# Optimization experiments

Measured on AMD Instinct MI355X. Metric: run time of the kernel, lower is better.

## Reference

```python
import jax, jax.numpy as jnp
import numpy as np

RMS_EPS = 1.1920928955078125e-07  # torch.finfo(float32).eps, nn.RMSNorm default when eps=None


def setup_inputs() -> dict:
    key = jax.random.key(0)
    ks = jax.random.split(key, 7)
    B, T, C, Wh, E, K = 8, 4096, 256, 1024, 8, 2
    return {
        "x": jax.random.normal(ks[0], (B, T, C), dtype=jnp.float32),
        "rms_weight": jnp.ones((C,), dtype=jnp.float32),
        "W1": jax.random.normal(ks[1], (E, C, Wh), dtype=jnp.float32),
        "b1": jax.random.normal(ks[2], (E, Wh), dtype=jnp.float32),
        "W2": jax.random.normal(ks[3], (E, Wh, C), dtype=jnp.float32),
        "b2": jax.random.normal(ks[4], (E, C), dtype=jnp.float32),
        "expert_ids": jax.random.randint(ks[5], (B, T, K), 0, E, dtype=jnp.int64),
    }


def reference(x, rms_weight, W1, b1, W2, b2, expert_ids):
    # RMSNorm over last dim (torch nn.RMSNorm, eps = float32 eps)
    xn = x * jax.lax.rsqrt(jnp.mean(x * x, axis=-1, keepdims=True) + RMS_EPS) * rms_weight
    # Per-expert 2-layer MLP. The torch code gathers per-token weight copies then bmm's;
    # mathematically identical (and far cheaper in memory) is: run every expert densely,
    # then gather the K selected expert outputs per token.
    h = jax.nn.gelu(jnp.einsum("btc,ecw->btew", xn, W1) + b1, approximate=False)  # [B,T,E,Wh]
    y = jnp.einsum("btew,ewc->btec", h, W2) + b2  # [B,T,E,C]
    # gather selected experts: [B,T,K,C]; dropout p is 0.0 (eval) -> identity
    out = jnp.take_along_axis(y, expert_ids[..., None], axis=2)
    return out
```

## Files before the change

### kernel.cpp

```cpp
#include <hip/hip_runtime.h>
#include <cstdint>

typedef unsigned short ushort_t;
typedef __bf16 bf16x8 __attribute__((ext_vector_type(8)));
typedef ushort_t u16x8 __attribute__((ext_vector_type(8)));
typedef float f32x4 __attribute__((ext_vector_type(4)));
typedef uint32_t u32x4 __attribute__((ext_vector_type(4)));

#define RMS_EPS 1.1920928955078125e-07f

__device__ __forceinline__ ushort_t f2bf(float f) {
  uint32_t u = __builtin_bit_cast(uint32_t, f);
  u += 0x7fffu + ((u >> 16) & 1u);
  return (ushort_t)(u >> 16);
}

__device__ __forceinline__ void g2l16(const ushort_t* g, ushort_t* l) {
  __builtin_amdgcn_global_load_lds(
      (const __attribute__((address_space(1))) uint32_t*)g,
      (__attribute__((address_space(3))) uint32_t*)l, 16, 0, 0);
}

__device__ __forceinline__ f32x4 mfma32(bf16x8 a, bf16x8 b, f32x4 c) {
  return __builtin_amdgcn_mfma_f32_16x16x32_bf16(a, b, c, 0, 0, 0);
}

__device__ __forceinline__ float gelu1(float v) {
  float vc = fminf(fmaxf(v, -2.9f), 2.9f);
  float x2 = vc * vc;
  float p = fmaf(-0.000414256f, x2, 0.0107517f);
  p = fmaf(p, x2, -0.1136149f);
  p = fmaf(p, x2, 0.786301f);
  float E = vc * p;
  float t = 0.5f * v;
  return fmaf(t, E, t);
}

__global__ void rmsnorm_cast(const float* __restrict__ x, const float* __restrict__ w,
                             ushort_t* __restrict__ xn) {
  int token = blockIdx.x * 4 + (threadIdx.x >> 6);
  int lane = threadIdx.x & 63;
  const float4* row = reinterpret_cast<const float4*>(x + (size_t)token * 256);
  float4 v = row[lane];
  float s = v.x * v.x + v.y * v.y + v.z * v.z + v.w * v.w;
#pragma unroll
  for (int off = 1; off < 64; off <<= 1) s += __shfl_xor(s, off);
  float inv = rsqrtf(s * (1.0f / 256.0f) + RMS_EPS);
  const float4* wr = reinterpret_cast<const float4*>(w);
  float4 wv = wr[lane];
  ushort4 o;
  o.x = f2bf(v.x * inv * wv.x);
  o.y = f2bf(v.y * inv * wv.y);
  o.z = f2bf(v.z * inv * wv.z);
  o.w = f2bf(v.w * inv * wv.w);
  *reinterpret_cast<ushort4*>(xn + (size_t)token * 256 + lane * 4) = o;
}

__global__ __launch_bounds__(256) void pack_w(const float* __restrict__ W1,
                                              const float* __restrict__ W2,
                                              ushort_t* __restrict__ w1f,
                                              ushort_t* __restrict__ w2f) {
  __shared__ ushort_t tile[64][130];
  int b = blockIdx.x;
  int isW2 = b >= 256;
  const float* src; ushort_t* dst; int e, kt, wt, rs;
  if (!isW2) { e = b >> 5; kt = (b >> 3) & 3; wt = b & 7; src = W1; dst = w1f; rs = 1024; }
  else { b -= 256; e = b >> 5; kt = (b >> 1) & 15; wt = b & 1; src = W2; dst = w2f; rs = 256; }
  int k0 = kt * 64, c0 = wt * 128;
  const float* sb = src + ((size_t)e << 18) + (size_t)k0 * rs + c0;
  int t = threadIdx.x;
#pragma unroll
  for (int i = 0; i < 8; ++i) {
    int f = i * 1024 + t * 4;
    int r = f >> 7, c = f & 127;
    float4 v = *reinterpret_cast<const float4*>(sb + (size_t)r * rs + c);
    ushort2 lo, hi;
    lo.x = f2bf(v.x); lo.y = f2bf(v.y); hi.x = f2bf(v.z); hi.y = f2bf(v.w);
    *reinterpret_cast<ushort2*>(&tile[r][c]) = lo;
    *reinterpret_cast<ushort2*>(&tile[r][c + 2]) = hi;
  }
  __syncthreads();
  int lane = t & 63, l16 = lane & 15, quad = lane >> 4;
  int wave = t >> 6;
  if (!isW2) {
#pragma unroll
    for (int p = 0; p < 4; ++p) {
      int u = p * 256 + t;
      int kk2 = (u >> 9) & 1;
      int rr = kk2 * 32 + quad * 8;
      int nt = (u >> 6) & 1, chL = (u >> 7) & 3;
      int cc = chL * 32 + nt * 16 + l16;
      u16x8 o;
#pragma unroll
      for (int j = 0; j < 8; ++j) o[j] = tile[rr + j][cc];
      size_t U = ((size_t)e * 32768) + (size_t)(wt * 4 + chL) * 1024 + (kt * 2 + kk2) * 128 + nt * 64 + lane;
      *reinterpret_cast<u16x8*>(dst + U * 8) = o;
    }
  } else {
#pragma unroll
    for (int p = 0; p < 4; ++p) {
      int u = p * 4 + wave;
      int chL = u >> 3, ctL = u & 7;
      int cc = ctL * 16 + l16;
      u16x8 o;
#pragma unroll
      for (int j = 0; j < 4; ++j) o[j] = tile[chL * 32 + quad * 4 + j][cc];
#pragma unroll
      for (int j = 0; j < 4; ++j) o[4 + j] = tile[chL * 32 + 16 + quad * 4 + j][cc];
      size_t U = (((size_t)(e * 32 + kt * 2 + chL) * 16) + (wt * 8 + ctL)) * 64 + lane;
      *reinterpret_cast<u16x8*>(dst + U * 8) = o;
    }
  }
}

__global__ void route_pairs(const int* __restrict__ eids, int* __restrict__ cnt,
                            int* __restrict__ lists) {
  __shared__ int lcnt[8], lbase[8];
  int tid = threadIdx.x;
  if (tid < 8) lcnt[tid] = 0;
  __syncthreads();
  int p = blockIdx.x * 256 + tid;
  int e = eids[p];
  int lpos = atomicAdd(&lcnt[e], 1);
  __syncthreads();
  if (tid < 8) lbase[tid] = atomicAdd(&cnt[tid], lcnt[tid]);
  __syncthreads();
  lists[e * 65536 + lbase[e] + lpos] = p;
}

__global__ __launch_bounds__(256, 3) void moe_mlp(
    const ushort_t* __restrict__ xn,
    const ushort_t* __restrict__ w1f,
    const ushort_t* __restrict__ w2f,
    const float* __restrict__ b1,
    const float* __restrict__ b2,
    const int* __restrict__ cnt,
    const int* __restrict__ lists,
    float* __restrict__ out)
{
  __shared__ __align__(16) ushort_t w1b[2][8192];
  __shared__ __align__(16) ushort_t w2b[8192];

  int nwg = gridDim.x;
  int q = nwg >> 3, r = nwg & 7;
  int xcd = blockIdx.x & 7, sub = blockIdx.x >> 3;
  int flat = (xcd < r ? xcd * (q + 1) : r * (q + 1) + (xcd - r) * q) + sub;

  int e = -1, tile = 0, accum = 0, n_e = 0;
#pragma unroll
  for (int i = 0; i < 8; ++i) {
    int c = cnt[i];
    int t = (c + 63) >> 6;
    if (e < 0 && flat < accum + t) { e = i; tile = flat - accum; n_e = c; }
    accum += t;
  }
  if (e < 0) return;
  int start = tile * 64;

  int tid = threadIdx.x;
  int wave = tid >> 6, lane = tid & 63, l16 = lane & 15, quad = lane >> 4;

  const ushort_t* w1e = w1f + ((size_t)e << 18);
  const ushort_t* w2e = w2f + ((size_t)e << 18);
  const int* le = lists + e * 65536;

  int gi = start + wave * 16 + l16;
  int pr = le[(gi < n_e) ? gi : 0];

#pragma unroll
  for (int j = 0; j < 4; ++j) {
    int p = j * 4 + wave;
    g2l16(w1e + p * 512 + lane * 8, &w1b[0][p * 512]);
  }

  bf16x8 afr[8];
  {
    const u32x4* ar = reinterpret_cast<const u32x4*>(xn + (size_t)(pr >> 1) * 256);
#pragma unroll
    for (int kk = 0; kk < 8; ++kk)
      afr[kk] = __builtin_bit_cast(bf16x8, ar[kk * 4 + quad]);
  }

  f32x4 acc[16];
#pragma unroll
  for (int ct = 0; ct < 16; ++ct) acc[ct] = (f32x4){0.f, 0.f, 0.f, 0.f};

  const float* b1e = b1 + e * 1024;

  for (int ch = 0; ch < 32; ++ch) {
    int cur = ch & 1;
    __syncthreads();

    {
      const ushort_t* n2 = w2e + ch * 8192;
#pragma unroll
      for (int j = 0; j < 4; ++j) {
        int p = j * 4 + wave;
        g2l16(n2 + p * 512 + lane * 8, &w2b[p * 512]);
      }
    }
    if (ch + 1 < 32) {
      const ushort_t* n1 = w1e + (ch + 1) * 8192;
#pragma unroll
      for (int j = 0; j < 4; ++j) {
        int p = j * 4 + wave;
        g2l16(n1 + p * 512 + lane * 8, &w1b[cur ^ 1][p * 512]);
      }
    }

    int w0 = ch * 32;
    f32x4 bia0 = *reinterpret_cast<const f32x4*>(b1e + w0 + quad * 4);
    f32x4 bia1 = *reinterpret_cast<const f32x4*>(b1e + w0 + 16 + quad * 4);

    const ushort_t* l1 = w1b[cur];
    f32x4 ht0 = (f32x4){0.f, 0.f, 0.f, 0.f};
    f32x4 ht1 = (f32x4){0.f, 0.f, 0.f, 0.f};
#pragma unroll
    for (int kk = 0; kk < 8; ++kk) {
      bf16x8 wA = *reinterpret_cast<const bf16x8*>(l1 + ((kk * 2 + 0) * 64 + lane) * 8);
      bf16x8 wB = *reinterpret_cast<const bf16x8*>(l1 + ((kk * 2 + 1) * 64 + lane) * 8);
      ht0 = mfma32(wA, afr[kk], ht0);
      ht1 = mfma32(wB, afr[kk], ht1);
    }

    u16x8 hp;
#pragma unroll
    for (int rr = 0; rr < 4; ++rr) {
      hp[rr]     = f2bf(gelu1(ht0[rr] + bia0[rr]));
      hp[4 + rr] = f2bf(gelu1(ht1[rr] + bia1[rr]));
    }
    bf16x8 hF = __builtin_bit_cast(bf16x8, hp);

    __syncthreads();

#pragma unroll
    for (int ct = 0; ct < 16; ++ct) {
      bf16x8 wq = *reinterpret_cast<const bf16x8*>(w2b + (ct * 64 + lane) * 8);
      acc[ct] = mfma32(wq, hF, acc[ct]);
    }
  }

  const float* b2e = b2 + e * 256;
  if (gi < n_e) {
    float* orow = out + (size_t)pr * 256;
#pragma unroll
    for (int ct = 0; ct < 16; ++ct) {
      f32x4 bv = *reinterpret_cast<const f32x4*>(b2e + ct * 16 + quad * 4);
      f32x4 o = acc[ct] + bv;
      *reinterpret_cast<f32x4*>(orow + ct * 16 + quad * 4) = o;
    }
  }
}

extern "C" void kernel_launch(void* const* d_in, const int* in_sizes, int n_in,
                              void* d_out, int out_size, void* d_ws, size_t ws_size,
                              hipStream_t stream) {
  const float* x  = (const float*)d_in[0];
  const float* rw = (const float*)d_in[1];
  const float* W1 = (const float*)d_in[2];
  const float* b1 = (const float*)d_in[3];
  const float* W2 = (const float*)d_in[4];
  const float* b2 = (const float*)d_in[5];
  const int* eids = (const int*)d_in[6];
  float* out = (float*)d_out;

  char* ws = (char*)d_ws;
  ushort_t* xn  = (ushort_t*)(ws);
  ushort_t* w1f = (ushort_t*)(ws + 16777216);
  ushort_t* w2f = (ushort_t*)(ws + 20971520);
  int* cnt      = (int*)(ws + 25165824);
  int* lists    = (int*)(ws + 25166080);

  hipMemsetAsync(cnt, 0, 8 * sizeof(int), stream);
  rmsnorm_cast<<<8192, 256, 0, stream>>>(x, rw, xn);
  pack_w<<<512, 256, 0, stream>>>(W1, W2, w1f, w2f);
  route_pairs<<<256, 256, 0, stream>>>(eids, cnt, lists);
  moe_mlp<<<1032, 256, 0, stream>>>(xn, w1f, w2f, b1, b2, cnt, lists, out);
}
```

Measured before the change: 224.6 us.

## Fuse preprocessing kernels and relax waits so W1 prefetch overlaps second GEMM

```diff
diff --git a/kernel.cpp b/kernel.cpp
--- a/kernel.cpp
+++ b/kernel.cpp
@@ -36,96 +36,96 @@
   return fmaf(t, E, t);
 }
 
-__global__ void rmsnorm_cast(const float* __restrict__ x, const float* __restrict__ w,
-                             ushort_t* __restrict__ xn) {
-  int token = blockIdx.x * 4 + (threadIdx.x >> 6);
-  int lane = threadIdx.x & 63;
-  const float4* row = reinterpret_cast<const float4*>(x + (size_t)token * 256);
-  float4 v = row[lane];
-  float s = v.x * v.x + v.y * v.y + v.z * v.z + v.w * v.w;
-#pragma unroll
-  for (int off = 1; off < 64; off <<= 1) s += __shfl_xor(s, off);
-  float inv = rsqrtf(s * (1.0f / 256.0f) + RMS_EPS);
-  const float4* wr = reinterpret_cast<const float4*>(w);
-  float4 wv = wr[lane];
-  ushort4 o;
-  o.x = f2bf(v.x * inv * wv.x);
-  o.y = f2bf(v.y * inv * wv.y);
-  o.z = f2bf(v.z * inv * wv.z);
-  o.w = f2bf(v.w * inv * wv.w);
-  *reinterpret_cast<ushort4*>(xn + (size_t)token * 256 + lane * 4) = o;
-}
-
-__global__ __launch_bounds__(256) void pack_w(const float* __restrict__ W1,
-                                              const float* __restrict__ W2,
-                                              ushort_t* __restrict__ w1f,
-                                              ushort_t* __restrict__ w2f) {
+__global__ __launch_bounds__(256) void fused_pre(
+    const float* __restrict__ x, const float* __restrict__ rw,
+    ushort_t* __restrict__ xn,
+    const float* __restrict__ W1, const float* __restrict__ W2,
+    ushort_t* __restrict__ w1f, ushort_t* __restrict__ w2f,
+    const int* __restrict__ eids, int* __restrict__ cnt,
+    int* __restrict__ lists) {
   __shared__ ushort_t tile[64][130];
-  int b = blockIdx.x;
-  int isW2 = b >= 256;
-  const float* src; ushort_t* dst; int e, kt, wt, rs;
-  if (!isW2) { e = b >> 5; kt = (b >> 3) & 3; wt = b & 7; src = W1; dst = w1f; rs = 1024; }
-  else { b -= 256; e = b >> 5; kt = (b >> 1) & 15; wt = b & 1; src = W2; dst = w2f; rs = 256; }
-  int k0 = kt * 64, c0 = wt * 128;
-  const float* sb = src + ((size_t)e << 18) + (size_t)k0 * rs + c0;
+  __shared__ int lcnt[8], lbase[8];
+  int bid = blockIdx.x;
   int t = threadIdx.x;
-#pragma unroll
-  for (int i = 0; i < 8; ++i) {
-    int f = i * 1024 + t * 4;
-    int r = f >> 7, c = f & 127;
-    float4 v = *reinterpret_cast<const float4*>(sb + (size_t)r * rs + c);
-    ushort2 lo, hi;
-    lo.x = f2bf(v.x); lo.y = f2bf(v.y); hi.x = f2bf(v.z); hi.y = f2bf(v.w);
-    *reinterpret_cast<ushort2*>(&tile[r][c]) = lo;
-    *reinterpret_cast<ushort2*>(&tile[r][c + 2]) = hi;
-  }
-  __syncthreads();
-  int lane = t & 63, l16 = lane & 15, quad = lane >> 4;
-  int wave = t >> 6;
-  if (!isW2) {
-#pragma unroll
-    for (int p = 0; p < 4; ++p) {
-      int u = p * 256 + t;
-      int kk2 = (u >> 9) & 1;
-      int rr = kk2 * 32 + quad * 8;
-      int nt = (u >> 6) & 1, chL = (u >> 7) & 3;
-      int cc = chL * 32 + nt * 16 + l16;
-      u16x8 o;
-#pragma unroll
-      for (int j = 0; j < 8; ++j) o[j] = tile[rr + j][cc];
-      size_t U = ((size_t)e * 32768) + (size_t)(wt * 4 + chL) * 1024 + (kt * 2 + kk2) * 128 + nt * 64 + lane;
-      *reinterpret_cast<u16x8*>(dst + U * 8) = o;
+
+  if (bid < 8192) {
+    int token = bid * 4 + (t >> 6);
+    int lane = t & 63;
+    const float4* row = reinterpret_cast<const float4*>(x + (size_t)token * 256);
+    float4 v = row[lane];
+    float s = v.x * v.x + v.y * v.y + v.z * v.z + v.w * v.w;
+#pragma unroll
+    for (int off = 1; off < 64; off <<= 1) s += __shfl_xor(s, off);
+    float inv = rsqrtf(s * (1.0f / 256.0f) + RMS_EPS);
+    const float4* wr = reinterpret_cast<const float4*>(rw);
+    float4 wv = wr[lane];
+    ushort4 o;
+    o.x = f2bf(v.x * inv * wv.x);
+    o.y = f2bf(v.y * inv * wv.y);
+    o.z = f2bf(v.z * inv * wv.z);
+    o.w = f2bf(v.w * inv * wv.w);
+    *reinterpret_cast<ushort4*>(xn + (size_t)token * 256 + lane * 4) = o;
+  } else if (bid < 8704) {
+    int b = bid - 8192;
+    int isW2 = b >= 256;
+    const float* src; ushort_t* dst; int e, kt, wt, rs;
+    if (!isW2) { e = b >> 5; kt = (b >> 3) & 3; wt = b & 7; src = W1; dst = w1f; rs = 1024; }
+    else { b -= 256; e = b >> 5; kt = (b >> 1) & 15; wt = b & 1; src = W2; dst = w2f; rs = 256; }
+    int k0 = kt * 64, c0 = wt * 128;
+    const float* sb = src + ((size_t)e << 18) + (size_t)k0 * rs + c0;
+#pragma unroll
+    for (int i = 0; i < 8; ++i) {
+      int f = i * 1024 + t * 4;
+      int r = f >> 7, c = f & 127;
+      float4 v = *reinterpret_cast<const float4*>(sb + (size_t)r * rs + c);
+      ushort2 lo, hi;
+      lo.x = f2bf(v.x); lo.y = f2bf(v.y); hi.x = f2bf(v.z); hi.y = f2bf(v.w);
+      *reinterpret_cast<ushort2*>(&tile[r][c]) = lo;
+      *reinterpret_cast<ushort2*>(&tile[r][c + 2]) = hi;
+    }
+    __syncthreads();
+    int lane = t & 63, l16 = lane & 15, quad = lane >> 4;
+    int wave = t >> 6;
+    if (!isW2) {
+#pragma unroll
+      for (int p = 0; p < 4; ++p) {
+        int u = p * 256 + t;
+        int kk2 = (u >> 9) & 1;
+        int rr = kk2 * 32 + quad * 8;
+        int nt = (u >> 6) & 1, chL = (u >> 7) & 3;
+        int cc = chL * 32 + nt * 16 + l16;
+        u16x8 o;
+#pragma unroll
+        for (int j = 0; j < 8; ++j) o[j] = tile[rr + j][cc];
+        size_t U = ((size_t)e * 32768) + (size_t)(wt * 4 + chL) * 1024 + (kt * 2 + kk2) * 128 + nt * 64 + lane;
+        *reinterpret_cast<u16x8*>(dst + U * 8) = o;
+      }
+    } else {
+#pragma unroll
+      for (int p = 0; p < 4; ++p) {
+        int u = p * 4 + wave;
+        int chL = u >> 3, ctL = u & 7;
+        int cc = ctL * 16 + l16;
+        u16x8 o;
+#pragma unroll
+        for (int j = 0; j < 4; ++j) o[j] = tile[chL * 32 + quad * 4 + j][cc];
+#pragma unroll
+        for (int j = 0; j < 4; ++j) o[4 + j] = tile[chL * 32 + 16 + quad * 4 + j][cc];
+        size_t U = (((size_t)(e * 32 + kt * 2 + chL) * 16) + (wt * 8 + ctL)) * 64 + lane;
+        *reinterpret_cast<u16x8*>(dst + U * 8) = o;
+      }
     }
   } else {
-#pragma unroll
-    for (int p = 0; p < 4; ++p) {
-      int u = p * 4 + wave;
-      int chL = u >> 3, ctL = u & 7;
-      int cc = ctL * 16 + l16;
-      u16x8 o;
-#pragma unroll
-      for (int j = 0; j < 4; ++j) o[j] = tile[chL * 32 + quad * 4 + j][cc];
-#pragma unroll
-      for (int j = 0; j < 4; ++j) o[4 + j] = tile[chL * 32 + 16 + quad * 4 + j][cc];
-      size_t U = (((size_t)(e * 32 + kt * 2 + chL) * 16) + (wt * 8 + ctL)) * 64 + lane;
-      *reinterpret_cast<u16x8*>(dst + U * 8) = o;
-    }
-  }
-}
-
-__global__ void route_pairs(const int* __restrict__ eids, int* __restrict__ cnt,
-                            int* __restrict__ lists) {
-  __shared__ int lcnt[8], lbase[8];
-  int tid = threadIdx.x;
-  if (tid < 8) lcnt[tid] = 0;
-  __syncthreads();
-  int p = blockIdx.x * 256 + tid;
-  int e = eids[p];
-  int lpos = atomicAdd(&lcnt[e], 1);
-  __syncthreads();
-  if (tid < 8) lbase[tid] = atomicAdd(&cnt[tid], lcnt[tid]);
-  __syncthreads();
-  lists[e * 65536 + lbase[e] + lpos] = p;
+    if (t < 8) lcnt[t] = 0;
+    __syncthreads();
+    int p = (bid - 8704) * 256 + t;
+    int e = eids[p];
+    int lpos = atomicAdd(&lcnt[e], 1);
+    __syncthreads();
+    if (t < 8) lbase[t] = atomicAdd(&cnt[t], lcnt[t]);
+    __syncthreads();
+    lists[e * 65536 + lbase[e] + lpos] = p;
+  }
 }
 
 __global__ __launch_bounds__(256, 3) void moe_mlp(
@@ -141,18 +141,16 @@
   __shared__ __align__(16) ushort_t w1b[2][8192];
   __shared__ __align__(16) ushort_t w2b[8192];
 
-  int nwg = gridDim.x;
-  int q = nwg >> 3, r = nwg & 7;
-  int xcd = blockIdx.x & 7, sub = blockIdx.x >> 3;
-  int flat = (xcd < r ? xcd * (q + 1) : r * (q + 1) + (xcd - r) * q) + sub;
+  int cpx = gridDim.x >> 3;
+  int flat = (blockIdx.x & 7) * cpx + (blockIdx.x >> 3);
 
   int e = -1, tile = 0, accum = 0, n_e = 0;
 #pragma unroll
   for (int i = 0; i < 8; ++i) {
     int c = cnt[i];
-    int t = (c + 63) >> 6;
-    if (e < 0 && flat < accum + t) { e = i; tile = flat - accum; n_e = c; }
-    accum += t;
+    int ti = (c + 63) >> 6;
+    if (e < 0 && flat < accum + ti) { e = i; tile = flat - accum; n_e = c; }
+    accum += ti;
   }
   if (e < 0) return;
   int start = tile * 64;
@@ -189,7 +187,14 @@
 
   for (int ch = 0; ch < 32; ++ch) {
     int cur = ch & 1;
-    __syncthreads();
+    asm volatile("s_waitcnt vmcnt(0)" ::: "memory");
+    __builtin_amdgcn_s_barrier();
+    __builtin_amdgcn_sched_barrier(0);
+
+    int w0 = ch * 32;
+    f32x4 bia0 = *reinterpret_cast<const f32x4*>(b1e + w0 + quad * 4);
+    f32x4 bia1 = *reinterpret_cast<const f32x4*>(b1e + w0 + 16 + quad * 4);
+    __builtin_amdgcn_sched_barrier(0);
 
     {
       const ushort_t* n2 = w2e + ch * 8192;
@@ -199,6 +204,7 @@
         g2l16(n2 + p * 512 + lane * 8, &w2b[p * 512]);
       }
     }
+    __builtin_amdgcn_sched_barrier(0);
     if (ch + 1 < 32) {
       const ushort_t* n1 = w1e + (ch + 1) * 8192;
 #pragma unroll
@@ -207,14 +213,12 @@
         g2l16(n1 + p * 512 + lane * 8, &w1b[cur ^ 1][p * 512]);
       }
     }
-
-    int w0 = ch * 32;
-    f32x4 bia0 = *reinterpret_cast<const f32x4*>(b1e + w0 + quad * 4);
-    f32x4 bia1 = *reinterpret_cast<const f32x4*>(b1e + w0 + 16 + quad * 4);
+    __builtin_amdgcn_sched_barrier(0);
 
     const ushort_t* l1 = w1b[cur];
     f32x4 ht0 = (f32x4){0.f, 0.f, 0.f, 0.f};
     f32x4 ht1 = (f32x4){0.f, 0.f, 0.f, 0.f};
+    __builtin_amdgcn_s_setprio(1);
 #pragma unroll
     for (int kk = 0; kk < 8; ++kk) {
       bf16x8 wA = *reinterpret_cast<const bf16x8*>(l1 + ((kk * 2 + 0) * 64 + lane) * 8);
@@ -222,6 +226,7 @@
       ht0 = mfma32(wA, afr[kk], ht0);
       ht1 = mfma32(wB, afr[kk], ht1);
     }
+    __builtin_amdgcn_s_setprio(0);
 
     u16x8 hp;
 #pragma unroll
@@ -231,13 +236,21 @@
     }
     bf16x8 hF = __builtin_bit_cast(bf16x8, hp);
 
-    __syncthreads();
-
+    if (ch < 31) {
+      asm volatile("s_waitcnt vmcnt(4)" ::: "memory");
+    } else {
+      asm volatile("s_waitcnt vmcnt(0)" ::: "memory");
+    }
+    __builtin_amdgcn_s_barrier();
+    __builtin_amdgcn_sched_barrier(0);
+
+    __builtin_amdgcn_s_setprio(1);
 #pragma unroll
     for (int ct = 0; ct < 16; ++ct) {
       bf16x8 wq = *reinterpret_cast<const bf16x8*>(w2b + (ct * 64 + lane) * 8);
       acc[ct] = mfma32(wq, hF, acc[ct]);
     }
+    __builtin_amdgcn_s_setprio(0);
   }
 
   const float* b2e = b2 + e * 256;
@@ -272,8 +285,6 @@
   int* lists    = (int*)(ws + 25166080);
 
   hipMemsetAsync(cnt, 0, 8 * sizeof(int), stream);
-  rmsnorm_cast<<<8192, 256, 0, stream>>>(x, rw, xn);
-  pack_w<<<512, 256, 0, stream>>>(W1, W2, w1f, w2f);
-  route_pairs<<<256, 256, 0, stream>>>(eids, cnt, lists);
+  fused_pre<<<8960, 256, 0, stream>>>(x, rw, xn, W1, W2, w1f, w2f, eids, cnt, lists);
   moe_mlp<<<1032, 256, 0, stream>>>(xn, w1f, w2f, b1, b2, cnt, lists, out);
 }
```

Measured after the change: 219.5 us. 1.02x faster.

## Fuse all stages into one persistent kernel with a grid-wide barrier

Applied to the files above, without the earlier changes.

```diff
diff --git a/kernel.cpp b/kernel.cpp
--- a/kernel.cpp
+++ b/kernel.cpp
@@ -36,218 +36,242 @@
   return fmaf(t, E, t);
 }
 
-__global__ void rmsnorm_cast(const float* __restrict__ x, const float* __restrict__ w,
-                             ushort_t* __restrict__ xn) {
-  int token = blockIdx.x * 4 + (threadIdx.x >> 6);
-  int lane = threadIdx.x & 63;
-  const float4* row = reinterpret_cast<const float4*>(x + (size_t)token * 256);
-  float4 v = row[lane];
-  float s = v.x * v.x + v.y * v.y + v.z * v.z + v.w * v.w;
-#pragma unroll
-  for (int off = 1; off < 64; off <<= 1) s += __shfl_xor(s, off);
-  float inv = rsqrtf(s * (1.0f / 256.0f) + RMS_EPS);
-  const float4* wr = reinterpret_cast<const float4*>(w);
-  float4 wv = wr[lane];
-  ushort4 o;
-  o.x = f2bf(v.x * inv * wv.x);
-  o.y = f2bf(v.y * inv * wv.y);
-  o.z = f2bf(v.z * inv * wv.z);
-  o.w = f2bf(v.w * inv * wv.w);
-  *reinterpret_cast<ushort4*>(xn + (size_t)token * 256 + lane * 4) = o;
-}
-
-__global__ __launch_bounds__(256) void pack_w(const float* __restrict__ W1,
-                                              const float* __restrict__ W2,
-                                              ushort_t* __restrict__ w1f,
-                                              ushort_t* __restrict__ w2f) {
-  __shared__ ushort_t tile[64][130];
-  int b = blockIdx.x;
-  int isW2 = b >= 256;
-  const float* src; ushort_t* dst; int e, kt, wt, rs;
-  if (!isW2) { e = b >> 5; kt = (b >> 3) & 3; wt = b & 7; src = W1; dst = w1f; rs = 1024; }
-  else { b -= 256; e = b >> 5; kt = (b >> 1) & 15; wt = b & 1; src = W2; dst = w2f; rs = 256; }
-  int k0 = kt * 64, c0 = wt * 128;
-  const float* sb = src + ((size_t)e << 18) + (size_t)k0 * rs + c0;
+union SmemU {
+  ushort_t tile[64][130];
+  struct {
+    ushort_t w1b[2][8192];
+    ushort_t w2b[8192];
+  } m;
+};
+
+__global__ __launch_bounds__(256, 2) void moe_all(
+    const float* __restrict__ x,
+    const float* __restrict__ rw,
+    ushort_t* __restrict__ xn,
+    const float* __restrict__ W1,
+    const float* __restrict__ W2,
+    ushort_t* __restrict__ w1f,
+    ushort_t* __restrict__ w2f,
+    const float* __restrict__ b1,
+    const float* __restrict__ b2,
+    const int* __restrict__ eids,
+    int* __restrict__ cnt,
+    int* __restrict__ bar,
+    int* __restrict__ lists,
+    float* __restrict__ out)
+{
+  __shared__ __align__(16) SmemU smem;
+  __shared__ int lcnt[8], lbase[8];
+
+  int bid = blockIdx.x;
   int t = threadIdx.x;
-#pragma unroll
-  for (int i = 0; i < 8; ++i) {
-    int f = i * 1024 + t * 4;
-    int r = f >> 7, c = f & 127;
-    float4 v = *reinterpret_cast<const float4*>(sb + (size_t)r * rs + c);
-    ushort2 lo, hi;
-    lo.x = f2bf(v.x); lo.y = f2bf(v.y); hi.x = f2bf(v.z); hi.y = f2bf(v.w);
-    *reinterpret_cast<ushort2*>(&tile[r][c]) = lo;
-    *reinterpret_cast<ushort2*>(&tile[r][c + 2]) = hi;
-  }
-  __syncthreads();
   int lane = t & 63, l16 = lane & 15, quad = lane >> 4;
   int wave = t >> 6;
-  if (!isW2) {
-#pragma unroll
-    for (int p = 0; p < 4; ++p) {
-      int u = p * 256 + t;
-      int kk2 = (u >> 9) & 1;
-      int rr = kk2 * 32 + quad * 8;
-      int nt = (u >> 6) & 1, chL = (u >> 7) & 3;
-      int cc = chL * 32 + nt * 16 + l16;
-      u16x8 o;
-#pragma unroll
-      for (int j = 0; j < 8; ++j) o[j] = tile[rr + j][cc];
-      size_t U = ((size_t)e * 32768) + (size_t)(wt * 4 + chL) * 1024 + (kt * 2 + kk2) * 128 + nt * 64 + lane;
-      *reinterpret_cast<u16x8*>(dst + U * 8) = o;
-    }
-  } else {
-#pragma unroll
-    for (int p = 0; p < 4; ++p) {
-      int u = p * 4 + wave;
-      int chL = u >> 3, ctL = u & 7;
-      int cc = ctL * 16 + l16;
-      u16x8 o;
-#pragma unroll
-      for (int j = 0; j < 4; ++j) o[j] = tile[chL * 32 + quad * 4 + j][cc];
-#pragma unroll
-      for (int j = 0; j < 4; ++j) o[4 + j] = tile[chL * 32 + 16 + quad * 4 + j][cc];
-      size_t U = (((size_t)(e * 32 + kt * 2 + chL) * 16) + (wt * 8 + ctL)) * 64 + lane;
-      *reinterpret_cast<u16x8*>(dst + U * 8) = o;
-    }
-  }
-}
-
-__global__ void route_pairs(const int* __restrict__ eids, int* __restrict__ cnt,
-                            int* __restrict__ lists) {
-  __shared__ int lcnt[8], lbase[8];
-  int tid = threadIdx.x;
-  if (tid < 8) lcnt[tid] = 0;
+
+  {
+    int b = bid;
+    int isW2 = b >= 256;
+    const float* src; ushort_t* dst; int e, kt, wt, rs;
+    if (!isW2) { e = b >> 5; kt = (b >> 3) & 3; wt = b & 7; src = W1; dst = w1f; rs = 1024; }
+    else { b -= 256; e = b >> 5; kt = (b >> 1) & 15; wt = b & 1; src = W2; dst = w2f; rs = 256; }
+    int k0 = kt * 64, c0 = wt * 128;
+    const float* sb = src + ((size_t)e << 18) + (size_t)k0 * rs + c0;
+#pragma unroll
+    for (int i = 0; i < 8; ++i) {
+      int f = i * 1024 + t * 4;
+      int r = f >> 7, c = f & 127;
+      float4 v = *reinterpret_cast<const float4*>(sb + (size_t)r * rs + c);
+      ushort2 lo, hi;
+      lo.x = f2bf(v.x); lo.y = f2bf(v.y); hi.x = f2bf(v.z); hi.y = f2bf(v.w);
+      *reinterpret_cast<ushort2*>(&smem.tile[r][c]) = lo;
+      *reinterpret_cast<ushort2*>(&smem.tile[r][c + 2]) = hi;
+    }
+    __syncthreads();
+    if (!isW2) {
+#pragma unroll
+      for (int p = 0; p < 4; ++p) {
+        int u = p * 256 + t;
+        int kk2 = (u >> 9) & 1;
+        int rr = kk2 * 32 + quad * 8;
+        int nt = (u >> 6) & 1, chL = (u >> 7) & 3;
+        int cc = chL * 32 + nt * 16 + l16;
+        u16x8 o;
+#pragma unroll
+        for (int j = 0; j < 8; ++j) o[j] = smem.tile[rr + j][cc];
+        size_t U = ((size_t)e * 32768) + (size_t)(wt * 4 + chL) * 1024 + (kt * 2 + kk2) * 128 + nt * 64 + lane;
+        *reinterpret_cast<u16x8*>(dst + U * 8) = o;
+      }
+    } else {
+#pragma unroll
+      for (int p = 0; p < 4; ++p) {
+        int u = p * 4 + wave;
+        int chL = u >> 3, ctL = u & 7;
+        int cc = ctL * 16 + l16;
+        u16x8 o;
+#pragma unroll
+        for (int j = 0; j < 4; ++j) o[j] = smem.tile[chL * 32 + quad * 4 + j][cc];
+#pragma unroll
+        for (int j = 0; j < 4; ++j) o[4 + j] = smem.tile[chL * 32 + 16 + quad * 4 + j][cc];
+        size_t U = (((size_t)(e * 32 + kt * 2 + chL) * 16) + (wt * 8 + ctL)) * 64 + lane;
+        *reinterpret_cast<u16x8*>(dst + U * 8) = o;
+      }
+    }
+  }
+
+#pragma unroll 1
+  for (int it = 0; it < 16; ++it) {
+    int token = bid * 64 + it * 4 + wave;
+    const float4* row = reinterpret_cast<const float4*>(x + (size_t)token * 256);
+    float4 v = row[lane];
+    float s = v.x * v.x + v.y * v.y + v.z * v.z + v.w * v.w;
+#pragma unroll
+    for (int off = 1; off < 64; off <<= 1) s += __shfl_xor(s, off);
+    float inv = rsqrtf(s * (1.0f / 256.0f) + RMS_EPS);
+    const float4* wr = reinterpret_cast<const float4*>(rw);
+    float4 wv = wr[lane];
+    ushort4 o;
+    o.x = f2bf(v.x * inv * wv.x);
+    o.y = f2bf(v.y * inv * wv.y);
+    o.z = f2bf(v.z * inv * wv.z);
+    o.w = f2bf(v.w * inv * wv.w);
+    *reinterpret_cast<ushort4*>(xn + (size_t)token * 256 + lane * 4) = o;
+  }
+
+  {
+    if (t < 8) lcnt[t] = 0;
+    __syncthreads();
+    int ee = 0, lpos = 0;
+    int p = bid * 128 + t;
+    if (t < 128) {
+      ee = eids[p];
+      lpos = atomicAdd(&lcnt[ee], 1);
+    }
+    __syncthreads();
+    if (t < 8) lbase[t] = atomicAdd(&cnt[t], lcnt[t]);
+    __syncthreads();
+    if (t < 128) lists[ee * 65536 + lbase[ee] + lpos] = p;
+  }
+
+  __threadfence();
   __syncthreads();
-  int p = blockIdx.x * 256 + tid;
-  int e = eids[p];
-  int lpos = atomicAdd(&lcnt[e], 1);
+  if (t == 0) {
+    __hip_atomic_fetch_add(bar, 1, __ATOMIC_ACQ_REL, __HIP_MEMORY_SCOPE_AGENT);
+    while (__hip_atomic_load(bar, __ATOMIC_ACQUIRE, __HIP_MEMORY_SCOPE_AGENT) < (int)gridDim.x) {
+      __builtin_amdgcn_s_sleep(8);
+    }
+  }
   __syncthreads();
-  if (tid < 8) lbase[tid] = atomicAdd(&cnt[tid], lcnt[tid]);
-  __syncthreads();
-  lists[e * 65536 + lbase[e] + lpos] = p;
-}
-
-__global__ __launch_bounds__(256, 3) void moe_mlp(
-    const ushort_t* __restrict__ xn,
-    const ushort_t* __restrict__ w1f,
-    const ushort_t* __restrict__ w2f,
-    const float* __restrict__ b1,
-    const float* __restrict__ b2,
-    const int* __restrict__ cnt,
-    const int* __restrict__ lists,
-    float* __restrict__ out)
-{
-  __shared__ __align__(16) ushort_t w1b[2][8192];
-  __shared__ __align__(16) ushort_t w2b[8192];
-
-  int nwg = gridDim.x;
-  int q = nwg >> 3, r = nwg & 7;
-  int xcd = blockIdx.x & 7, sub = blockIdx.x >> 3;
-  int flat = (xcd < r ? xcd * (q + 1) : r * (q + 1) + (xcd - r) * q) + sub;
-
-  int e = -1, tile = 0, accum = 0, n_e = 0;
-#pragma unroll
-  for (int i = 0; i < 8; ++i) {
-    int c = cnt[i];
-    int t = (c + 63) >> 6;
-    if (e < 0 && flat < accum + t) { e = i; tile = flat - accum; n_e = c; }
-    accum += t;
-  }
-  if (e < 0) return;
-  int start = tile * 64;
-
-  int tid = threadIdx.x;
-  int wave = tid >> 6, lane = tid & 63, l16 = lane & 15, quad = lane >> 4;
-
-  const ushort_t* w1e = w1f + ((size_t)e << 18);
-  const ushort_t* w2e = w2f + ((size_t)e << 18);
-  const int* le = lists + e * 65536;
-
-  int gi = start + wave * 16 + l16;
-  int pr = le[(gi < n_e) ? gi : 0];
-
-#pragma unroll
-  for (int j = 0; j < 4; ++j) {
-    int p = j * 4 + wave;
-    g2l16(w1e + p * 512 + lane * 8, &w1b[0][p * 512]);
-  }
-
-  bf16x8 afr[8];
-  {
-    const u32x4* ar = reinterpret_cast<const u32x4*>(xn + (size_t)(pr >> 1) * 256);
-#pragma unroll
-    for (int kk = 0; kk < 8; ++kk)
-      afr[kk] = __builtin_bit_cast(bf16x8, ar[kk * 4 + quad]);
-  }
-
-  f32x4 acc[16];
-#pragma unroll
-  for (int ct = 0; ct < 16; ++ct) acc[ct] = (f32x4){0.f, 0.f, 0.f, 0.f};
-
-  const float* b1e = b1 + e * 1024;
-
-  for (int ch = 0; ch < 32; ++ch) {
-    int cur = ch & 1;
-    __syncthreads();
-
+
+  int cnt_l[8];
+#pragma unroll
+  for (int i = 0; i < 8; ++i)
+    cnt_l[i] = __hip_atomic_load(&cnt[i], __ATOMIC_ACQUIRE, __HIP_MEMORY_SCOPE_AGENT);
+
+#pragma unroll 1
+  for (int v = bid; v < 1032; v += 512) {
+    int flat = (v & 7) * 129 + (v >> 3);
+
+    int e = -1, tile = 0, accum = 0, n_e = 0;
+#pragma unroll
+    for (int i = 0; i < 8; ++i) {
+      int c = cnt_l[i];
+      int ti = (c + 63) >> 6;
+      if (e < 0 && flat < accum + ti) { e = i; tile = flat - accum; n_e = c; }
+      accum += ti;
+    }
+    if (e < 0) continue;
+    int start = tile * 64;
+
+    const ushort_t* w1e = w1f + ((size_t)e << 18);
+    const ushort_t* w2e = w2f + ((size_t)e << 18);
+    const int* le = lists + e * 65536;
+
+    int gi = start + wave * 16 + l16;
+    int pr = le[(gi < n_e) ? gi : 0];
+
+#pragma unroll
+    for (int j = 0; j < 4; ++j) {
+      int p = j * 4 + wave;
+      g2l16(w1e + p * 512 + lane * 8, &smem.m.w1b[0][p * 512]);
+    }
+
+    bf16x8 afr[8];
     {
-      const ushort_t* n2 = w2e + ch * 8192;
-#pragma unroll
-      for (int j = 0; j < 4; ++j) {
-        int p = j * 4 + wave;
-        g2l16(n2 + p * 512 + lane * 8, &w2b[p * 512]);
-      }
-    }
-    if (ch + 1 < 32) {
-      const ushort_t* n1 = w1e + (ch + 1) * 8192;
-#pragma unroll
-      for (int j = 0; j < 4; ++j) {
-        int p = j * 4 + wave;
-        g2l16(n1 + p * 512 + lane * 8, &w1b[cur ^ 1][p * 512]);
-      }
-    }
-
-    int w0 = ch * 32;
-    f32x4 bia0 = *reinterpret_cast<const f32x4*>(b1e + w0 + quad * 4);
-    f32x4 bia1 = *reinterpret_cast<const f32x4*>(b1e + w0 + 16 + quad * 4);
-
-    const ushort_t* l1 = w1b[cur];
-    f32x4 ht0 = (f32x4){0.f, 0.f, 0.f, 0.f};
-    f32x4 ht1 = (f32x4){0.f, 0.f, 0.f, 0.f};
-#pragma unroll
-    for (int kk = 0; kk < 8; ++kk) {
-      bf16x8 wA = *reinterpret_cast<const bf16x8*>(l1 + ((kk * 2 + 0) * 64 + lane) * 8);
-      bf16x8 wB = *reinterpret_cast<const bf16x8*>(l1 + ((kk * 2 + 1) * 64 + lane) * 8);
-      ht0 = mfma32(wA, afr[kk], ht0);
-      ht1 = mfma32(wB, afr[kk], ht1);
-    }
-
-    u16x8 hp;
-#pragma unroll
-    for (int rr = 0; rr < 4; ++rr) {
-      hp[rr]     = f2bf(gelu1(ht0[rr] + bia0[rr]));
-      hp[4 + rr] = f2bf(gelu1(ht1[rr] + bia1[rr]));
-    }
-    bf16x8 hF = __builtin_bit_cast(bf16x8, hp);
-
-    __syncthreads();
-
-#pragma unroll
-    for (int ct = 0; ct < 16; ++ct) {
-      bf16x8 wq = *reinterpret_cast<const bf16x8*>(w2b + (ct * 64 + lane) * 8);
-      acc[ct] = mfma32(wq, hF, acc[ct]);
-    }
-  }
-
-  const float* b2e = b2 + e * 256;
-  if (gi < n_e) {
-    float* orow = out + (size_t)pr * 256;
-#pragma unroll
-    for (int ct = 0; ct < 16; ++ct) {
-      f32x4 bv = *reinterpret_cast<const f32x4*>(b2e + ct * 16 + quad * 4);
-      f32x4 o = acc[ct] + bv;
-      *reinterpret_cast<f32x4*>(orow + ct * 16 + quad * 4) = o;
+      const u32x4* ar = reinterpret_cast<const u32x4*>(xn + (size_t)(pr >> 1) * 256);
+#pragma unroll
+      for (int kk = 0; kk < 8; ++kk)
+        afr[kk] = __builtin_bit_cast(bf16x8, ar[kk * 4 + quad]);
+    }
+
+    f32x4 acc[16];
+#pragma unroll
+    for (int ct = 0; ct < 16; ++ct) acc[ct] = (f32x4){0.f, 0.f, 0.f, 0.f};
+
+    const float* b1e = b1 + e * 1024;
+
+#pragma unroll 1
+    for (int ch = 0; ch < 32; ++ch) {
+      int cur = ch & 1;
+      __syncthreads();
+
+      {
+        const ushort_t* n2 = w2e + ch * 8192;
+#pragma unroll
+        for (int j = 0; j < 4; ++j) {
+          int p = j * 4 + wave;
+          g2l16(n2 + p * 512 + lane * 8, &smem.m.w2b[p * 512]);
+        }
+      }
+      if (ch + 1 < 32) {
+        const ushort_t* n1 = w1e + (ch + 1) * 8192;
+#pragma unroll
+        for (int j = 0; j < 4; ++j) {
+          int p = j * 4 + wave;
+          g2l16(n1 + p * 512 + lane * 8, &smem.m.w1b[cur ^ 1][p * 512]);
+        }
+      }
+
+      const ushort_t* l1 = smem.m.w1b[cur];
+      f32x4 ht0 = (f32x4){0.f, 0.f, 0.f, 0.f};
+      f32x4 ht1 = (f32x4){0.f, 0.f, 0.f, 0.f};
+#pragma unroll
+      for (int kk = 0; kk < 8; ++kk) {
+        bf16x8 wA = *reinterpret_cast<const bf16x8*>(l1 + ((kk * 2 + 0) * 64 + lane) * 8);
+        bf16x8 wB = *reinterpret_cast<const bf16x8*>(l1 + ((kk * 2 + 1) * 64 + lane) * 8);
+        ht0 = mfma32(wA, afr[kk], ht0);
+        ht1 = mfma32(wB, afr[kk], ht1);
+      }
+
+      int w0 = ch * 32;
+      f32x4 bia0 = *reinterpret_cast<const f32x4*>(b1e + w0 + quad * 4);
+      f32x4 bia1 = *reinterpret_cast<const f32x4*>(b1e + w0 + 16 + quad * 4);
+
+      u16x8 hp;
+#pragma unroll
+      for (int rr = 0; rr < 4; ++rr) {
+        hp[rr]     = f2bf(gelu1(ht0[rr] + bia0[rr]));
+        hp[4 + rr] = f2bf(gelu1(ht1[rr] + bia1[rr]));
+      }
+      bf16x8 hF = __builtin_bit_cast(bf16x8, hp);
+
+      __syncthreads();
+
+#pragma unroll
+      for (int ct = 0; ct < 16; ++ct) {
+        bf16x8 wq = *reinterpret_cast<const bf16x8*>(smem.m.w2b + (ct * 64 + lane) * 8);
+        acc[ct] = mfma32(wq, hF, acc[ct]);
+      }
+    }
+
+    const float* b2e = b2 + e * 256;
+    if (gi < n_e) {
+      float* orow = out + (size_t)pr * 256;
+#pragma unroll
+      for (int ct = 0; ct < 16; ++ct) {
+        f32x4 bv = *reinterpret_cast<const f32x4*>(b2e + ct * 16 + quad * 4);
+        f32x4 o = acc[ct] + bv;
+        *reinterpret_cast<f32x4*>(orow + ct * 16 + quad * 4) = o;
+      }
     }
   }
 }
@@ -269,11 +293,10 @@
   ushort_t* w1f = (ushort_t*)(ws + 16777216);
   ushort_t* w2f = (ushort_t*)(ws + 20971520);
   int* cnt      = (int*)(ws + 25165824);
+  int* bar      = (int*)(ws + 25165824 + 64);
   int* lists    = (int*)(ws + 25166080);
 
-  hipMemsetAsync(cnt, 0, 8 * sizeof(int), stream);
-  rmsnorm_cast<<<8192, 256, 0, stream>>>(x, rw, xn);
-  pack_w<<<512, 256, 0, stream>>>(W1, W2, w1f, w2f);
-  route_pairs<<<256, 256, 0, stream>>>(eids, cnt, lists);
-  moe_mlp<<<1032, 256, 0, stream>>>(xn, w1f, w2f, b1, b2, cnt, lists, out);
-}
+  hipMemsetAsync(cnt, 0, 256, stream);
+  moe_all<<<512, 256, 0, stream>>>(x, rw, xn, W1, W2, w1f, w2f, b1, b2,
+                                   eids, cnt, bar, lists, out);
+}
```

Result: slower. 472.1 us (+110.2%).
